# Kernel optimization log

Hardware: AMD Instinct MI355X
Metric: run time of the kernel (lower is better)

The kernel has to match this reference:

```python
import jax, jax.numpy as jnp
from jax import lax
import numpy as np

HEADS = 3
DIM_HEAD = 64
INNER = HEADS * DIM_HEAD  # 192
SCALE = DIM_HEAD ** -0.5
BN_EPS = 1e-5


def _sep_conv(x, dw, gamma, beta, mean, var, pw, stride):
    """Depthwise conv (SAME) -> BatchNorm (inference) -> 1x1 pointwise conv."""
    C = x.shape[-1]
    x = lax.conv_general_dilated(
        x, dw, window_strides=(stride, stride), padding='SAME',
        dimension_numbers=('NHWC', 'HWIO', 'NHWC'), feature_group_count=C)
    x = (x - mean) * lax.rsqrt(var + BN_EPS) * gamma + beta
    return jnp.einsum('bhwc,cd->bhwd', x, pw)


def setup_inputs() -> dict:
    key = jax.random.key(0)
    ks = jax.random.split(key, 8)
    B, H, W, C = 8, 56, 56, 192
    return {
        'x': jax.random.normal(ks[0], (B, H, W, C), dtype=jnp.float32),
        'dw_q': jax.random.normal(ks[1], (3, 3, 1, C), dtype=jnp.float32) * 0.1,
        'q_gamma': jnp.ones((C,), jnp.float32),
        'q_beta': jnp.zeros((C,), jnp.float32),
        'q_mean': jnp.zeros((C,), jnp.float32),
        'q_var': jnp.ones((C,), jnp.float32),
        'pw_q': jax.random.normal(ks[2], (C, INNER), dtype=jnp.float32) / np.sqrt(C).astype(np.float32),
        'dw_kv': jax.random.normal(ks[3], (3, 3, 1, C), dtype=jnp.float32) * 0.1,
        'kv_gamma': jnp.ones((C,), jnp.float32),
        'kv_beta': jnp.zeros((C,), jnp.float32),
        'kv_mean': jnp.zeros((C,), jnp.float32),
        'kv_var': jnp.ones((C,), jnp.float32),
        'pw_kv': jax.random.normal(ks[4], (C, 2 * INNER), dtype=jnp.float32) / np.sqrt(C).astype(np.float32),
        'out_w': jax.random.normal(ks[5], (INNER, C), dtype=jnp.float32) / np.sqrt(INNER).astype(np.float32),
        'out_b': jnp.zeros((C,), jnp.float32),
    }


def reference(x, dw_q, q_gamma, q_beta, q_mean, q_var, pw_q,
              dw_kv, kv_gamma, kv_beta, kv_mean, kv_var, pw_kv,
              out_w, out_b):
    B, H, W, C = x.shape
    q = _sep_conv(x, dw_q, q_gamma, q_beta, q_mean, q_var, pw_q, 1)      # [B,H,W,INNER]
    kv = _sep_conv(x, dw_kv, kv_gamma, kv_beta, kv_mean, kv_var, pw_kv, 2)  # [B,H/2,W/2,2*INNER]
    k, v = jnp.split(kv, 2, axis=-1)

    def split_heads(t):
        b, h, w, _ = t.shape
        return t.reshape(b, h * w, HEADS, DIM_HEAD)

    q, k, v = split_heads(q), split_heads(k), split_heads(v)  # [B,N,h,d]
    scores = jnp.einsum('bihd,bjhd->bhij', q, k) * SCALE       # [B,h,Nq,Nkv]
    attn = jax.nn.softmax(scores, axis=-1)
    o = jnp.einsum('bhij,bjhd->bihd', attn, v)                 # [B,Nq,h,d]
    o = o.reshape(B, H, W, INNER)
    return jnp.einsum('bhwc,cd->bhwd', o, out_w) + out_b
```

## Files before the change

### kernel.cpp

```cpp
#include <hip/hip_runtime.h>
#include <hip/hip_bf16.h>

namespace {
constexpr int Bb = 8, Hh = 56, Ww = 56, Cc = 192;
constexpr int NQ  = Hh * Ww;
constexpr int NKV = 28 * 28;
constexpr float EPS = 1e-5f;
constexpr float QSCALE = 0.125f * 1.4426950408889634f;
}

typedef __attribute__((ext_vector_type(8))) short          bf16x8;
typedef __attribute__((ext_vector_type(4))) float          f32x4;
typedef __attribute__((ext_vector_type(8))) unsigned short u16x8;

__device__ inline unsigned short f2b(float f) {
  __hip_bfloat16 h = __float2bfloat16(f);
  return __builtin_bit_cast(unsigned short, h);
}

__device__ inline uint2 pack4(float a, float b, float c, float d) {
  uint2 r;
  r.x = (unsigned)f2b(a) | ((unsigned)f2b(b) << 16);
  r.y = (unsigned)f2b(c) | ((unsigned)f2b(d) << 16);
  return r;
}

__device__ inline void dwbn_body(
    int idx, const float* __restrict__ x, const float* __restrict__ w,
    const float* __restrict__ gamma, const float* __restrict__ beta,
    const float* __restrict__ mean, const float* __restrict__ var,
    unsigned short* __restrict__ out, int OH, int OW, int stride, int pad)
{
  int c4 = idx % 48;
  int t = idx / 48;
  int ow = t % OW; t /= OW;
  int oh = t % OH; int b = t / OH;
  const int c = c4 * 4;

  float4 acc = make_float4(0.f, 0.f, 0.f, 0.f);
#pragma unroll
  for (int kh = 0; kh < 3; ++kh) {
    int ih = oh * stride - pad + kh;
    if (ih < 0 || ih >= Hh) continue;
#pragma unroll
    for (int kw = 0; kw < 3; ++kw) {
      int iw = ow * stride - pad + kw;
      if (iw < 0 || iw >= Ww) continue;
      float4 xv = *(const float4*)&x[((size_t)(b * Hh + ih) * Ww + iw) * Cc + c];
      float4 wv = *(const float4*)&w[(kh * 3 + kw) * Cc + c];
      acc.x += xv.x * wv.x; acc.y += xv.y * wv.y;
      acc.z += xv.z * wv.z; acc.w += xv.w * wv.w;
    }
  }
  float4 gm = *(const float4*)&gamma[c];
  float4 bt = *(const float4*)&beta[c];
  float4 mn = *(const float4*)&mean[c];
  float4 vr = *(const float4*)&var[c];
  float r0 = (acc.x - mn.x) * gm.x / sqrtf(vr.x + EPS) + bt.x;
  float r1 = (acc.y - mn.y) * gm.y / sqrtf(vr.y + EPS) + bt.y;
  float r2 = (acc.z - mn.z) * gm.z / sqrtf(vr.z + EPS) + bt.z;
  float r3 = (acc.w - mn.w) * gm.w / sqrtf(vr.w + EPS) + bt.w;
  const size_t row = (size_t)(b * OH + oh) * OW + ow;
  *reinterpret_cast<uint2*>(&out[row * 192 + c]) = pack4(r0, r1, r2, r3);
}

__global__ __launch_bounds__(256) void stage1_kernel(
    const float* __restrict__ x,
    const float* __restrict__ dw_q, const float* __restrict__ q_gamma,
    const float* __restrict__ q_beta, const float* __restrict__ q_mean,
    const float* __restrict__ q_var,
    const float* __restrict__ dw_kv, const float* __restrict__ kv_gamma,
    const float* __restrict__ kv_beta, const float* __restrict__ kv_mean,
    const float* __restrict__ kv_var,
    const float* __restrict__ pwq, const float* __restrict__ pwkv,
    const float* __restrict__ outw,
    unsigned short* __restrict__ dwq, unsigned short* __restrict__ dwkv,
    unsigned short* __restrict__ wq, unsigned short* __restrict__ wkv,
    unsigned short* __restrict__ wo)
{
  const int blk = blockIdx.x;
  if (blk < 4704) {
    dwbn_body(blk * 256 + threadIdx.x, x, dw_q, q_gamma, q_beta, q_mean, q_var,
              dwq, 56, 56, 1, 1);
  } else if (blk < 5880) {
    dwbn_body((blk - 4704) * 256 + threadIdx.x, x, dw_kv, kv_gamma, kv_beta,
              kv_mean, kv_var, dwkv, 28, 28, 2, 0);
  } else {
    int i = (blk - 5880) * 256 + threadIdx.x;
    if (i < 36864) {
      int n = i / 192, k = i - n * 192;
      wq[i] = f2b(pwq[k * 192 + n]);
    } else if (i < 110592) {
      int j = i - 36864;
      int n = j / 192, k = j - n * 192;
      wkv[j] = f2b(pwkv[k * 384 + n]);
    } else {
      int j = i - 110592;
      int n = j / 192, k = j - n * 192;
      wo[j] = f2b(outw[k * 192 + n]);
    }
  }
}

__global__ __launch_bounds__(256) void gemm_qkv_kernel(
    const unsigned short* __restrict__ dwq, const unsigned short* __restrict__ dwkv,
    const unsigned short* __restrict__ Wq, const unsigned short* __restrict__ Wkv,
    unsigned short* __restrict__ Qbuf, unsigned short* __restrict__ Kbuf,
    unsigned short* __restrict__ Vtbuf)
{
  __shared__ unsigned short As[128][72];
  __shared__ unsigned short Bs[64][72];

  const int blk = blockIdx.x;
  const bool isQ = blk < 588;
  const int lb = isQ ? blk : blk - 588;
  const unsigned short* __restrict__ A  = isQ ? dwq : dwkv;
  const unsigned short* __restrict__ Bt = isQ ? Wq : Wkv;
  const int nbl = isQ ? 3 : 6;
  const int NR  = isQ ? 3136 : 784;

  const int bm = lb / nbl, bn = lb % nbl;
  const int row0 = bm << 7, col0 = bn << 6;
  const int tid = threadIdx.x;
  const int lane = tid & 63, w = tid >> 6;
  const int lr = lane & 15, lg = lane >> 4;
  const int wm = w >> 1, wn = w & 1;

  f32x4 acc[4][2];
#pragma unroll
  for (int mr = 0; mr < 4; ++mr)
#pragma unroll
    for (int nr = 0; nr < 2; ++nr) acc[mr][nr] = (f32x4){0.f, 0.f, 0.f, 0.f};

  for (int k0 = 0; k0 < 192; k0 += 64) {
    {
      const int r = tid >> 1, c0 = (tid & 1) * 32;
      const unsigned short* src = A + (size_t)(row0 + r) * 192 + k0 + c0;
#pragma unroll
      for (int u = 0; u < 4; ++u)
        *(u16x8*)&As[r][c0 + u * 8] = *(const u16x8*)&src[u * 8];
    }
    {
      const int n = tid >> 2, c0 = (tid & 3) * 16;
      const unsigned short* src = Bt + (size_t)(col0 + n) * 192 + k0 + c0;
#pragma unroll
      for (int u = 0; u < 2; ++u)
        *(u16x8*)&Bs[n][c0 + u * 8] = *(const u16x8*)&src[u * 8];
    }
    __syncthreads();
#pragma unroll
    for (int ks = 0; ks < 2; ++ks) {
      bf16x8 a[4], b[2];
#pragma unroll
      for (int mr = 0; mr < 4; ++mr)
        a[mr] = *(const bf16x8*)&As[wm * 64 + mr * 16 + lr][ks * 32 + lg * 8];
#pragma unroll
      for (int nr = 0; nr < 2; ++nr)
        b[nr] = *(const bf16x8*)&Bs[wn * 32 + nr * 16 + lr][ks * 32 + lg * 8];
#pragma unroll
      for (int mr = 0; mr < 4; ++mr)
#pragma unroll
        for (int nr = 0; nr < 2; ++nr)
          acc[mr][nr] = __builtin_amdgcn_mfma_f32_16x16x32_bf16(a[mr], b[nr], acc[mr][nr], 0, 0, 0);
    }
    __syncthreads();
  }

#pragma unroll
  for (int mr = 0; mr < 4; ++mr) {
#pragma unroll
    for (int nr = 0; nr < 2; ++nr) {
      const int c = col0 + wn * 32 + nr * 16 + lr;
      const int rbase = row0 + wm * 64 + mr * 16 + lg * 4;
      if (isQ) {
        const int h = c >> 6, d = c & 63;
        const int b = rbase / 3136;
        const int n0 = rbase - b * 3136;
#pragma unroll
        for (int j = 0; j < 4; ++j)
          Qbuf[(((size_t)b * 3 + h) * 3136 + n0 + j) * 64 + d] = f2b(acc[mr][nr][j] * QSCALE);
      } else if (c < 192) {
        const int h = c >> 6, d = c & 63;
        const int b = rbase / 784;
        const int n0 = rbase - b * 784;
#pragma unroll
        for (int j = 0; j < 4; ++j)
          Kbuf[(((size_t)b * 3 + h) * 784 + n0 + j) * 64 + d] = f2b(acc[mr][nr][j]);
      } else {
        const int h = (c - 192) >> 6, d = (c - 192) & 63;
        const int b = rbase / 784;
        const int n0 = rbase - b * 784;
        uint2 v = pack4(acc[mr][nr][0], acc[mr][nr][1], acc[mr][nr][2], acc[mr][nr][3]);
        *reinterpret_cast<uint2*>(&Vtbuf[(((size_t)b * 3 + h) * 64 + d) * 784 + n0]) = v;
      }
    }
  }
}

__global__ __launch_bounds__(256) void gemm_out_kernel(
    const unsigned short* __restrict__ A, const unsigned short* __restrict__ Bt,
    const float* __restrict__ bias, float* __restrict__ O32)
{
  __shared__ unsigned short As[128][72];
  __shared__ unsigned short Bs[64][72];

  const int bm = blockIdx.x / 3, bn = blockIdx.x % 3;
  const int row0 = bm << 7, col0 = bn << 6;
  const int tid = threadIdx.x;
  const int lane = tid & 63, w = tid >> 6;
  const int lr = lane & 15, lg = lane >> 4;
  const int wm = w >> 1, wn = w & 1;

  f32x4 acc[4][2];
#pragma unroll
  for (int mr = 0; mr < 4; ++mr)
#pragma unroll
    for (int nr = 0; nr < 2; ++nr) acc[mr][nr] = (f32x4){0.f, 0.f, 0.f, 0.f};

  for (int k0 = 0; k0 < 192; k0 += 64) {
    {
      const int r = tid >> 1, c0 = (tid & 1) * 32;
      const unsigned short* src = A + (size_t)(row0 + r) * 192 + k0 + c0;
#pragma unroll
      for (int u = 0; u < 4; ++u)
        *(u16x8*)&As[r][c0 + u * 8] = *(const u16x8*)&src[u * 8];
    }
    {
      const int n = tid >> 2, c0 = (tid & 3) * 16;
      const unsigned short* src = Bt + (size_t)(col0 + n) * 192 + k0 + c0;
#pragma unroll
      for (int u = 0; u < 2; ++u)
        *(u16x8*)&Bs[n][c0 + u * 8] = *(const u16x8*)&src[u * 8];
    }
    __syncthreads();
#pragma unroll
    for (int ks = 0; ks < 2; ++ks) {
      bf16x8 a[4], b[2];
#pragma unroll
      for (int mr = 0; mr < 4; ++mr)
        a[mr] = *(const bf16x8*)&As[wm * 64 + mr * 16 + lr][ks * 32 + lg * 8];
#pragma unroll
      for (int nr = 0; nr < 2; ++nr)
        b[nr] = *(const bf16x8*)&Bs[wn * 32 + nr * 16 + lr][ks * 32 + lg * 8];
#pragma unroll
      for (int mr = 0; mr < 4; ++mr)
#pragma unroll
        for (int nr = 0; nr < 2; ++nr)
          acc[mr][nr] = __builtin_amdgcn_mfma_f32_16x16x32_bf16(a[mr], b[nr], acc[mr][nr], 0, 0, 0);
    }
    __syncthreads();
  }

#pragma unroll
  for (int mr = 0; mr < 4; ++mr) {
#pragma unroll
    for (int nr = 0; nr < 2; ++nr) {
      const int c = col0 + wn * 32 + nr * 16 + lr;
      const int rbase = row0 + wm * 64 + mr * 16 + lg * 4;
      const float bb = bias[c];
#pragma unroll
      for (int j = 0; j < 4; ++j)
        O32[(size_t)(rbase + j) * 192 + c] = acc[mr][nr][j] + bb;
    }
  }
}

__global__ __launch_bounds__(256) void attn_mfma_kernel(
    const unsigned short* __restrict__ Qb, const unsigned short* __restrict__ Kb,
    const unsigned short* __restrict__ Vtb, unsigned short* __restrict__ Ob)
{
  __shared__ unsigned short Ks[64][72];
  __shared__ unsigned short Vts[64][72];
  __shared__ unsigned short Ps[64][72];
  __shared__ float ls[4][16];

  const int blk = blockIdx.x;
  const int qt = blk % 49;
  const int bh = blk / 49;
  const int n0 = qt * 64;
  const int tid = threadIdx.x;
  const int lane = tid & 63;
  const int w = tid >> 6;
  const int lr = lane & 15, lg = lane >> 4;
  const int srow = w * 16 + lr;
  const int scc  = lg;

  const unsigned short* qrow = Qb + ((size_t)bh * NQ + n0 + w * 16 + lr) * 64;
  const bf16x8 aq0 = *(const bf16x8*)&qrow[lg * 8];
  const bf16x8 aq1 = *(const bf16x8*)&qrow[32 + lg * 8];

  const unsigned short* kbase = Kb + (size_t)bh * NKV * 64;
  const unsigned short* vrow  = Vtb + ((size_t)bh * 64 + srow) * NKV;

  u16x8 kr0, kr1, vr0, vr1;
  {
    const unsigned short* kp = kbase + (size_t)srow * 64;
    kr0 = *(const u16x8*)&kp[scc * 8];
    kr1 = *(const u16x8*)&kp[scc * 8 + 32];
    vr0 = *(const u16x8*)&vrow[scc * 8];
    vr1 = *(const u16x8*)&vrow[scc * 8 + 32];
  }
  *(u16x8*)&Ks[srow][scc * 8]       = kr0;
  *(u16x8*)&Ks[srow][scc * 8 + 32]  = kr1;
  *(u16x8*)&Vts[srow][scc * 8]      = vr0;
  *(u16x8*)&Vts[srow][scc * 8 + 32] = vr1;
  __syncthreads();

  f32x4 oacc[4];
#pragma unroll
  for (int db = 0; db < 4; ++db) oacc[db] = (f32x4){0.f, 0.f, 0.f, 0.f};
  float lsum = 0.f;

  for (int kt = 0; kt < 12; ++kt) {
    {
      const int nk = kt + 1;
      const int kvg = (nk * 64 + srow < NKV) ? nk * 64 + srow : NKV - 1;
      const unsigned short* kp = kbase + (size_t)kvg * 64;
      kr0 = *(const u16x8*)&kp[scc * 8];
      kr1 = *(const u16x8*)&kp[scc * 8 + 32];
      const int vb = nk * 64 + scc * 8;
      const int vc0 = (vb      <= NKV - 8) ? vb      : NKV - 8;
      const int vc1 = (vb + 32 <= NKV - 8) ? vb + 32 : NKV - 8;
      vr0 = *(const u16x8*)&vrow[vc0];
      vr1 = *(const u16x8*)&vrow[vc1];
    }

    f32x4 st[4];
#pragma unroll
    for (int nb = 0; nb < 4; ++nb) {
      const bf16x8 bk0 = *(const bf16x8*)&Ks[nb * 16 + lr][lg * 8];
      const bf16x8 bk1 = *(const bf16x8*)&Ks[nb * 16 + lr][32 + lg * 8];
      f32x4 a = (f32x4){0.f, 0.f, 0.f, 0.f};
      a = __builtin_amdgcn_mfma_f32_16x16x32_bf16(bk0, aq0, a, 0, 0, 0);
      a = __builtin_amdgcn_mfma_f32_16x16x32_bf16(bk1, aq1, a, 0, 0, 0);
      st[nb] = a;
    }

#pragma unroll
    for (int nb = 0; nb < 4; ++nb) {
      float p[4];
#pragma unroll
      for (int r = 0; r < 4; ++r) p[r] = exp2f(st[nb][r]);
      lsum += (p[0] + p[1]) + (p[2] + p[3]);
      uint2 u = pack4(p[0], p[1], p[2], p[3]);
      *reinterpret_cast<uint2*>(&Ps[w * 16 + lr][nb * 16 + lg * 4]) = u;
    }

    const bf16x8 pa0 = *(const bf16x8*)&Ps[w * 16 + lr][lg * 8];
    const bf16x8 pa1 = *(const bf16x8*)&Ps[w * 16 + lr][32 + lg * 8];
#pragma unroll
    for (int db = 0; db < 4; ++db) {
      const bf16x8 vb0 = *(const bf16x8*)&Vts[db * 16 + lr][lg * 8];
      const bf16x8 vb1 = *(const bf16x8*)&Vts[db * 16 + lr][32 + lg * 8];
      oacc[db] = __builtin_amdgcn_mfma_f32_16x16x32_bf16(pa0, vb0, oacc[db], 0, 0, 0);
      oacc[db] = __builtin_amdgcn_mfma_f32_16x16x32_bf16(pa1, vb1, oacc[db], 0, 0, 0);
    }

    __syncthreads();
    *(u16x8*)&Ks[srow][scc * 8]       = kr0;
    *(u16x8*)&Ks[srow][scc * 8 + 32]  = kr1;
    *(u16x8*)&Vts[srow][scc * 8]      = vr0;
    *(u16x8*)&Vts[srow][scc * 8 + 32] = vr1;
    __syncthreads();
  }

  {
    const bf16x8 bk0 = *(const bf16x8*)&Ks[lr][lg * 8];
    const bf16x8 bk1 = *(const bf16x8*)&Ks[lr][32 + lg * 8];
    f32x4 a = (f32x4){0.f, 0.f, 0.f, 0.f};
    a = __builtin_amdgcn_mfma_f32_16x16x32_bf16(bk0, aq0, a, 0, 0, 0);
    a = __builtin_amdgcn_mfma_f32_16x16x32_bf16(bk1, aq1, a, 0, 0, 0);
    float p[4];
#pragma unroll
    for (int r = 0; r < 4; ++r) p[r] = exp2f(a[r]);
    lsum += (p[0] + p[1]) + (p[2] + p[3]);
    *reinterpret_cast<uint2*>(&Ps[w * 16 + lr][lg * 4]) = pack4(p[0], p[1], p[2], p[3]);
    uint2 z; z.x = 0u; z.y = 0u;
    *reinterpret_cast<uint2*>(&Ps[w * 16 + lr][16 + lg * 4]) = z;
    const bf16x8 pa0 = *(const bf16x8*)&Ps[w * 16 + lr][lg * 8];
#pragma unroll
    for (int db = 0; db < 4; ++db) {
      const bf16x8 vb0 = *(const bf16x8*)&Vts[db * 16 + lr][lg * 8];
      oacc[db] = __builtin_amdgcn_mfma_f32_16x16x32_bf16(pa0, vb0, oacc[db], 0, 0, 0);
    }
  }

  float l = lsum;
  l += __shfl_xor(l, 16);
  l += __shfl_xor(l, 32);
  if (lg == 0) ls[w][lr] = l;
  const float4 lv = *(const float4*)&ls[w][lg * 4];

  const int b = bh / 3, h = bh - b * 3;
  float linv[4];
#pragma unroll
  for (int j = 0; j < 4; ++j) linv[j] = 1.f / ((&lv.x)[j]);
#pragma unroll
  for (int j = 0; j < 4; ++j) {
    const int qg = n0 + w * 16 + lg * 4 + j;
    unsigned short* orow = Ob + ((size_t)b * NQ + qg) * 192 + h * 64 + lr;
#pragma unroll
    for (int db = 0; db < 4; ++db) orow[db * 16] = f2b(oacc[db][j] * linv[j]);
  }
}

extern "C" void kernel_launch(void* const* d_in, const int* in_sizes, int n_in,
                              void* d_out, int out_size, void* d_ws, size_t ws_size,
                              hipStream_t stream)
{
  const float* x        = (const float*)d_in[0];
  const float* dw_q     = (const float*)d_in[1];
  const float* q_gamma  = (const float*)d_in[2];
  const float* q_beta   = (const float*)d_in[3];
  const float* q_mean   = (const float*)d_in[4];
  const float* q_var    = (const float*)d_in[5];
  const float* pw_q     = (const float*)d_in[6];
  const float* dw_kv    = (const float*)d_in[7];
  const float* kv_gamma = (const float*)d_in[8];
  const float* kv_beta  = (const float*)d_in[9];
  const float* kv_mean  = (const float*)d_in[10];
  const float* kv_var   = (const float*)d_in[11];
  const float* pw_kv    = (const float*)d_in[12];
  const float* out_w    = (const float*)d_in[13];
  const float* out_b    = (const float*)d_in[14];
  float* out = (float*)d_out;

  unsigned short* dwq   = (unsigned short*)d_ws;
  unsigned short* dwkv  = dwq   + (size_t)25088 * 192;
  unsigned short* Qbuf  = dwkv  + (size_t)6272 * 192;
  unsigned short* Kbuf  = Qbuf  + (size_t)24 * 3136 * 64;
  unsigned short* Vtbuf = Kbuf  + (size_t)24 * 784 * 64;
  unsigned short* Wq    = Vtbuf + (size_t)24 * 784 * 64;
  unsigned short* Wkv   = Wq + 36864;
  unsigned short* Wo    = Wkv + 73728;

  stage1_kernel<<<6456, 256, 0, stream>>>(
      x, dw_q, q_gamma, q_beta, q_mean, q_var,
      dw_kv, kv_gamma, kv_beta, kv_mean, kv_var,
      pw_q, pw_kv, out_w, dwq, dwkv, Wq, Wkv, Wo);
  gemm_qkv_kernel<<<882, 256, 0, stream>>>(dwq, dwkv, Wq, Wkv, Qbuf, Kbuf, Vtbuf);
  attn_mfma_kernel<<<8 * 3 * 49, 256, 0, stream>>>(Qbuf, Kbuf, Vtbuf, dwq);
  gemm_out_kernel<<<588, 256, 0, stream>>>(dwq, Wo, out_b, out);
}
```

Before: 89.00 us.

## Fuse depthwise conv+BN into QKV pointwise GEMM via shared-memory A tile

New measurement: 125.6 us. +41.1%, slower.

```diff
diff --git a/kernel.cpp b/kernel.cpp
--- a/kernel.cpp
+++ b/kernel.cpp
@@ -25,46 +25,28 @@
   return r;
 }
 
-__device__ inline void dwbn_body(
-    int idx, const float* __restrict__ x, const float* __restrict__ w,
-    const float* __restrict__ gamma, const float* __restrict__ beta,
-    const float* __restrict__ mean, const float* __restrict__ var,
-    unsigned short* __restrict__ out, int OH, int OW, int stride, int pad)
+__global__ __launch_bounds__(256) void prep_w_kernel(
+    const float* __restrict__ pwq, const float* __restrict__ pwkv,
+    const float* __restrict__ outw,
+    unsigned short* __restrict__ wq, unsigned short* __restrict__ wkv,
+    unsigned short* __restrict__ wo)
 {
-  int c4 = idx % 48;
-  int t = idx / 48;
-  int ow = t % OW; t /= OW;
-  int oh = t % OH; int b = t / OH;
-  const int c = c4 * 4;
-
-  float4 acc = make_float4(0.f, 0.f, 0.f, 0.f);
-#pragma unroll
-  for (int kh = 0; kh < 3; ++kh) {
-    int ih = oh * stride - pad + kh;
-    if (ih < 0 || ih >= Hh) continue;
-#pragma unroll
-    for (int kw = 0; kw < 3; ++kw) {
-      int iw = ow * stride - pad + kw;
-      if (iw < 0 || iw >= Ww) continue;
-      float4 xv = *(const float4*)&x[((size_t)(b * Hh + ih) * Ww + iw) * Cc + c];
-      float4 wv = *(const float4*)&w[(kh * 3 + kw) * Cc + c];
-      acc.x += xv.x * wv.x; acc.y += xv.y * wv.y;
-      acc.z += xv.z * wv.z; acc.w += xv.w * wv.w;
-    }
-  }
-  float4 gm = *(const float4*)&gamma[c];
-  float4 bt = *(const float4*)&beta[c];
-  float4 mn = *(const float4*)&mean[c];
-  float4 vr = *(const float4*)&var[c];
-  float r0 = (acc.x - mn.x) * gm.x / sqrtf(vr.x + EPS) + bt.x;
-  float r1 = (acc.y - mn.y) * gm.y / sqrtf(vr.y + EPS) + bt.y;
-  float r2 = (acc.z - mn.z) * gm.z / sqrtf(vr.z + EPS) + bt.z;
-  float r3 = (acc.w - mn.w) * gm.w / sqrtf(vr.w + EPS) + bt.w;
-  const size_t row = (size_t)(b * OH + oh) * OW + ow;
-  *reinterpret_cast<uint2*>(&out[row * 192 + c]) = pack4(r0, r1, r2, r3);
-}
-
-__global__ __launch_bounds__(256) void stage1_kernel(
+  int i = blockIdx.x * 256 + threadIdx.x;
+  if (i < 36864) {
+    int n = i / 192, k = i - n * 192;
+    wq[i] = f2b(pwq[k * 192 + n]);
+  } else if (i < 110592) {
+    int j = i - 36864;
+    int n = j / 192, k = j - n * 192;
+    wkv[j] = f2b(pwkv[k * 384 + n]);
+  } else if (i < 147456) {
+    int j = i - 110592;
+    int n = j / 192, k = j - n * 192;
+    wo[j] = f2b(outw[k * 192 + n]);
+  }
+}
+
+__global__ __launch_bounds__(256) void dwgemm_kernel(
     const float* __restrict__ x,
     const float* __restrict__ dw_q, const float* __restrict__ q_gamma,
     const float* __restrict__ q_beta, const float* __restrict__ q_mean,
@@ -72,126 +54,123 @@
     const float* __restrict__ dw_kv, const float* __restrict__ kv_gamma,
     const float* __restrict__ kv_beta, const float* __restrict__ kv_mean,
     const float* __restrict__ kv_var,
-    const float* __restrict__ pwq, const float* __restrict__ pwkv,
-    const float* __restrict__ outw,
-    unsigned short* __restrict__ dwq, unsigned short* __restrict__ dwkv,
-    unsigned short* __restrict__ wq, unsigned short* __restrict__ wkv,
-    unsigned short* __restrict__ wo)
-{
-  const int blk = blockIdx.x;
-  if (blk < 4704) {
-    dwbn_body(blk * 256 + threadIdx.x, x, dw_q, q_gamma, q_beta, q_mean, q_var,
-              dwq, 56, 56, 1, 1);
-  } else if (blk < 5880) {
-    dwbn_body((blk - 4704) * 256 + threadIdx.x, x, dw_kv, kv_gamma, kv_beta,
-              kv_mean, kv_var, dwkv, 28, 28, 2, 0);
-  } else {
-    int i = (blk - 5880) * 256 + threadIdx.x;
-    if (i < 36864) {
-      int n = i / 192, k = i - n * 192;
-      wq[i] = f2b(pwq[k * 192 + n]);
-    } else if (i < 110592) {
-      int j = i - 36864;
-      int n = j / 192, k = j - n * 192;
-      wkv[j] = f2b(pwkv[k * 384 + n]);
-    } else {
-      int j = i - 110592;
-      int n = j / 192, k = j - n * 192;
-      wo[j] = f2b(outw[k * 192 + n]);
-    }
-  }
-}
-
-__global__ __launch_bounds__(256) void gemm_qkv_kernel(
-    const unsigned short* __restrict__ dwq, const unsigned short* __restrict__ dwkv,
     const unsigned short* __restrict__ Wq, const unsigned short* __restrict__ Wkv,
     unsigned short* __restrict__ Qbuf, unsigned short* __restrict__ Kbuf,
     unsigned short* __restrict__ Vtbuf)
 {
-  __shared__ unsigned short As[128][72];
-  __shared__ unsigned short Bs[64][72];
+  __shared__ unsigned short As[64][200];
+  __shared__ unsigned short Bs[192][72];
 
   const int blk = blockIdx.x;
-  const bool isQ = blk < 588;
-  const int lb = isQ ? blk : blk - 588;
-  const unsigned short* __restrict__ A  = isQ ? dwq : dwkv;
-  const unsigned short* __restrict__ Bt = isQ ? Wq : Wkv;
-  const int nbl = isQ ? 3 : 6;
-  const int NR  = isQ ? 3136 : 784;
-
-  const int bm = lb / nbl, bn = lb % nbl;
-  const int row0 = bm << 7, col0 = bn << 6;
+  const bool isQ = blk < 392;
+  const int lb = isQ ? blk : blk - 392;
+  const int bn = isQ ? 0 : lb / 98;
+  const int row0 = (isQ ? lb : (lb % 98)) * 64;
+
+  const float* dww = isQ ? dw_q : dw_kv;
+  const float* gmp = isQ ? q_gamma : kv_gamma;
+  const float* btp = isQ ? q_beta  : kv_beta;
+  const float* mnp = isQ ? q_mean  : kv_mean;
+  const float* vrp = isQ ? q_var   : kv_var;
+  const unsigned short* Btw = isQ ? Wq : (Wkv + (size_t)bn * 192 * 192);
+  const int OH = isQ ? 56 : 28, OW = isQ ? 56 : 28;
+  const int stride = isQ ? 1 : 2, pad = isQ ? 1 : 0;
+  const int NR = isQ ? 3136 : 784;
+
   const int tid = threadIdx.x;
+
+#pragma unroll
+  for (int it = 0; it < 12; ++it) {
+    const int task = it * 256 + tid;
+    const int c4 = task % 48, r = task / 48;
+    const int p = row0 + r;
+    const int b = p / NR;
+    const int rem = p - b * NR;
+    const int oh = rem / OW, ow = rem - oh * OW;
+    const int c = c4 * 4;
+
+    float4 acc = make_float4(0.f, 0.f, 0.f, 0.f);
+#pragma unroll
+    for (int kh = 0; kh < 3; ++kh) {
+      const int ih = oh * stride - pad + kh;
+      if (ih < 0 || ih >= Hh) continue;
+#pragma unroll
+      for (int kw = 0; kw < 3; ++kw) {
+        const int iw = ow * stride - pad + kw;
+        if (iw < 0 || iw >= Ww) continue;
+        float4 xv = *(const float4*)&x[((size_t)(b * Hh + ih) * Ww + iw) * Cc + c];
+        float4 wv = *(const float4*)&dww[(kh * 3 + kw) * Cc + c];
+        acc.x += xv.x * wv.x; acc.y += xv.y * wv.y;
+        acc.z += xv.z * wv.z; acc.w += xv.w * wv.w;
+      }
+    }
+    float4 gm = *(const float4*)&gmp[c];
+    float4 bt = *(const float4*)&btp[c];
+    float4 mn = *(const float4*)&mnp[c];
+    float4 vr = *(const float4*)&vrp[c];
+    float r0 = (acc.x - mn.x) * gm.x / sqrtf(vr.x + EPS) + bt.x;
+    float r1 = (acc.y - mn.y) * gm.y / sqrtf(vr.y + EPS) + bt.y;
+    float r2 = (acc.z - mn.z) * gm.z / sqrtf(vr.z + EPS) + bt.z;
+    float r3 = (acc.w - mn.w) * gm.w / sqrtf(vr.w + EPS) + bt.w;
+    *reinterpret_cast<uint2*>(&As[r][c]) = pack4(r0, r1, r2, r3);
+  }
+
   const int lane = tid & 63, w = tid >> 6;
   const int lr = lane & 15, lg = lane >> 4;
   const int wm = w >> 1, wn = w & 1;
 
-  f32x4 acc[4][2];
-#pragma unroll
-  for (int mr = 0; mr < 4; ++mr)
-#pragma unroll
-    for (int nr = 0; nr < 2; ++nr) acc[mr][nr] = (f32x4){0.f, 0.f, 0.f, 0.f};
+  f32x4 acc[2][6];
+#pragma unroll
+  for (int mr = 0; mr < 2; ++mr)
+#pragma unroll
+    for (int nr = 0; nr < 6; ++nr) acc[mr][nr] = (f32x4){0.f, 0.f, 0.f, 0.f};
 
   for (int k0 = 0; k0 < 192; k0 += 64) {
-    {
-      const int r = tid >> 1, c0 = (tid & 1) * 32;
-      const unsigned short* src = A + (size_t)(row0 + r) * 192 + k0 + c0;
-#pragma unroll
-      for (int u = 0; u < 4; ++u)
-        *(u16x8*)&As[r][c0 + u * 8] = *(const u16x8*)&src[u * 8];
-    }
-    {
-      const int n = tid >> 2, c0 = (tid & 3) * 16;
-      const unsigned short* src = Bt + (size_t)(col0 + n) * 192 + k0 + c0;
-#pragma unroll
-      for (int u = 0; u < 2; ++u)
-        *(u16x8*)&Bs[n][c0 + u * 8] = *(const u16x8*)&src[u * 8];
+    __syncthreads();
+#pragma unroll
+    for (int it = 0; it < 6; ++it) {
+      const int task = it * 256 + tid;
+      const int n = task >> 3, c8 = task & 7;
+      *(u16x8*)&Bs[n][c8 * 8] = *(const u16x8*)&Btw[(size_t)n * 192 + k0 + c8 * 8];
     }
     __syncthreads();
 #pragma unroll
     for (int ks = 0; ks < 2; ++ks) {
-      bf16x8 a[4], b[2];
-#pragma unroll
-      for (int mr = 0; mr < 4; ++mr)
-        a[mr] = *(const bf16x8*)&As[wm * 64 + mr * 16 + lr][ks * 32 + lg * 8];
-#pragma unroll
-      for (int nr = 0; nr < 2; ++nr)
-        b[nr] = *(const bf16x8*)&Bs[wn * 32 + nr * 16 + lr][ks * 32 + lg * 8];
-#pragma unroll
-      for (int mr = 0; mr < 4; ++mr)
-#pragma unroll
-        for (int nr = 0; nr < 2; ++nr)
+      bf16x8 a[2], b[6];
+#pragma unroll
+      for (int mr = 0; mr < 2; ++mr)
+        a[mr] = *(const bf16x8*)&As[wm * 32 + mr * 16 + lr][k0 + ks * 32 + lg * 8];
+#pragma unroll
+      for (int nr = 0; nr < 6; ++nr)
+        b[nr] = *(const bf16x8*)&Bs[wn * 96 + nr * 16 + lr][ks * 32 + lg * 8];
+#pragma unroll
+      for (int mr = 0; mr < 2; ++mr)
+#pragma unroll
+        for (int nr = 0; nr < 6; ++nr)
           acc[mr][nr] = __builtin_amdgcn_mfma_f32_16x16x32_bf16(a[mr], b[nr], acc[mr][nr], 0, 0, 0);
     }
-    __syncthreads();
-  }
-
-#pragma unroll
-  for (int mr = 0; mr < 4; ++mr) {
-#pragma unroll
-    for (int nr = 0; nr < 2; ++nr) {
-      const int c = col0 + wn * 32 + nr * 16 + lr;
-      const int rbase = row0 + wm * 64 + mr * 16 + lg * 4;
+  }
+
+#pragma unroll
+  for (int mr = 0; mr < 2; ++mr) {
+#pragma unroll
+    for (int nr = 0; nr < 6; ++nr) {
+      const int c = wn * 96 + nr * 16 + lr;
+      const int rbase = row0 + wm * 32 + mr * 16 + lg * 4;
+      const int h = c >> 6, d = c & 63;
+      const int b = rbase / NR;
+      const int n0r = rbase - b * NR;
       if (isQ) {
-        const int h = c >> 6, d = c & 63;
-        const int b = rbase / 3136;
-        const int n0 = rbase - b * 3136;
 #pragma unroll
         for (int j = 0; j < 4; ++j)
-          Qbuf[(((size_t)b * 3 + h) * 3136 + n0 + j) * 64 + d] = f2b(acc[mr][nr][j] * QSCALE);
-      } else if (c < 192) {
-        const int h = c >> 6, d = c & 63;
-        const int b = rbase / 784;
-        const int n0 = rbase - b * 784;
+          Qbuf[(((size_t)b * 3 + h) * 3136 + n0r + j) * 64 + d] = f2b(acc[mr][nr][j] * QSCALE);
+      } else if (bn == 0) {
 #pragma unroll
         for (int j = 0; j < 4; ++j)
-          Kbuf[(((size_t)b * 3 + h) * 784 + n0 + j) * 64 + d] = f2b(acc[mr][nr][j]);
+          Kbuf[(((size_t)b * 3 + h) * 784 + n0r + j) * 64 + d] = f2b(acc[mr][nr][j]);
       } else {
-        const int h = (c - 192) >> 6, d = (c - 192) & 63;
-        const int b = rbase / 784;
-        const int n0 = rbase - b * 784;
         uint2 v = pack4(acc[mr][nr][0], acc[mr][nr][1], acc[mr][nr][2], acc[mr][nr][3]);
-        *reinterpret_cast<uint2*>(&Vtbuf[(((size_t)b * 3 + h) * 64 + d) * 784 + n0]) = v;
+        *reinterpret_cast<uint2*>(&Vtbuf[(((size_t)b * 3 + h) * 64 + d) * 784 + n0r]) = v;
       }
     }
   }
@@ -425,20 +404,19 @@
   const float* out_b    = (const float*)d_in[14];
   float* out = (float*)d_out;
 
-  unsigned short* dwq   = (unsigned short*)d_ws;
-  unsigned short* dwkv  = dwq   + (size_t)25088 * 192;
-  unsigned short* Qbuf  = dwkv  + (size_t)6272 * 192;
+  unsigned short* Obuf  = (unsigned short*)d_ws;
+  unsigned short* Qbuf  = Obuf  + (size_t)25088 * 192;
   unsigned short* Kbuf  = Qbuf  + (size_t)24 * 3136 * 64;
   unsigned short* Vtbuf = Kbuf  + (size_t)24 * 784 * 64;
   unsigned short* Wq    = Vtbuf + (size_t)24 * 784 * 64;
   unsigned short* Wkv   = Wq + 36864;
   unsigned short* Wo    = Wkv + 73728;
 
-  stage1_kernel<<<6456, 256, 0, stream>>>(
+  prep_w_kernel<<<576, 256, 0, stream>>>(pw_q, pw_kv, out_w, Wq, Wkv, Wo);
+  dwgemm_kernel<<<588, 256, 0, stream>>>(
       x, dw_q, q_gamma, q_beta, q_mean, q_var,
       dw_kv, kv_gamma, kv_beta, kv_mean, kv_var,
-      pw_q, pw_kv, out_w, dwq, dwkv, Wq, Wkv, Wo);
-  gemm_qkv_kernel<<<882, 256, 0, stream>>>(dwq, dwkv, Wq, Wkv, Qbuf, Kbuf, Vtbuf);
-  attn_mfma_kernel<<<8 * 3 * 49, 256, 0, stream>>>(Qbuf, Kbuf, Vtbuf, dwq);
-  gemm_out_kernel<<<588, 256, 0, stream>>>(dwq, Wo, out_b, out);
-}
+      Wq, Wkv, Qbuf, Kbuf, Vtbuf);
+  attn_mfma_kernel<<<8 * 3 * 49, 256, 0, stream>>>(Qbuf, Kbuf, Vtbuf, Obuf);
+  gemm_out_kernel<<<588, 256, 0, stream>>>(Obuf, Wo, out_b, out);
+}
```

## Process 128 queries per attention block to reuse K/V tiles across two row groups

Applied to the files above, without the earlier changes.

Measured after the change: 91.45 us. +2.7%, slower.

```diff
diff --git a/kernel.cpp b/kernel.cpp
--- a/kernel.cpp
+++ b/kernel.cpp
@@ -271,13 +271,13 @@
 {
   __shared__ unsigned short Ks[64][72];
   __shared__ unsigned short Vts[64][72];
-  __shared__ unsigned short Ps[64][72];
-  __shared__ float ls[4][16];
+  __shared__ unsigned short Ps[128][72];
+  __shared__ float ls[4][2][16];
 
   const int blk = blockIdx.x;
-  const int qt = blk % 49;
-  const int bh = blk / 49;
-  const int n0 = qt * 64;
+  const int qt = blk % 25;
+  const int bh = blk / 25;
+  const int n0 = qt * 128;
   const int tid = threadIdx.x;
   const int lane = tid & 63;
   const int w = tid >> 6;
@@ -285,9 +285,14 @@
   const int srow = w * 16 + lr;
   const int scc  = lg;
 
-  const unsigned short* qrow = Qb + ((size_t)bh * NQ + n0 + w * 16 + lr) * 64;
-  const bf16x8 aq0 = *(const bf16x8*)&qrow[lg * 8];
-  const bf16x8 aq1 = *(const bf16x8*)&qrow[32 + lg * 8];
+  const int qrA = n0 + w * 32 + lr;
+  const int qrB = qrA + 16;
+  const unsigned short* qpA = Qb + ((size_t)bh * NQ + (qrA < NQ ? qrA : NQ - 1)) * 64;
+  const unsigned short* qpB = Qb + ((size_t)bh * NQ + (qrB < NQ ? qrB : NQ - 1)) * 64;
+  const bf16x8 qa0 = *(const bf16x8*)&qpA[lg * 8];
+  const bf16x8 qa1 = *(const bf16x8*)&qpA[32 + lg * 8];
+  const bf16x8 qb0 = *(const bf16x8*)&qpB[lg * 8];
+  const bf16x8 qb1 = *(const bf16x8*)&qpB[32 + lg * 8];
 
   const unsigned short* kbase = Kb + (size_t)bh * NKV * 64;
   const unsigned short* vrow  = Vtb + ((size_t)bh * 64 + srow) * NKV;
@@ -306,10 +311,16 @@
   *(u16x8*)&Vts[srow][scc * 8 + 32] = vr1;
   __syncthreads();
 
-  f32x4 oacc[4];
-#pragma unroll
-  for (int db = 0; db < 4; ++db) oacc[db] = (f32x4){0.f, 0.f, 0.f, 0.f};
-  float lsum = 0.f;
+  f32x4 oaccA[4], oaccB[4];
+#pragma unroll
+  for (int db = 0; db < 4; ++db) {
+    oaccA[db] = (f32x4){0.f, 0.f, 0.f, 0.f};
+    oaccB[db] = (f32x4){0.f, 0.f, 0.f, 0.f};
+  }
+  float lsumA = 0.f, lsumB = 0.f;
+
+  const int rowA = w * 32 + lr;
+  const int rowB = rowA + 16;
 
   for (int kt = 0; kt < 12; ++kt) {
     {
@@ -325,35 +336,44 @@
       vr1 = *(const u16x8*)&vrow[vc1];
     }
 
-    f32x4 st[4];
+    f32x4 stA[4], stB[4];
 #pragma unroll
     for (int nb = 0; nb < 4; ++nb) {
       const bf16x8 bk0 = *(const bf16x8*)&Ks[nb * 16 + lr][lg * 8];
       const bf16x8 bk1 = *(const bf16x8*)&Ks[nb * 16 + lr][32 + lg * 8];
       f32x4 a = (f32x4){0.f, 0.f, 0.f, 0.f};
-      a = __builtin_amdgcn_mfma_f32_16x16x32_bf16(bk0, aq0, a, 0, 0, 0);
-      a = __builtin_amdgcn_mfma_f32_16x16x32_bf16(bk1, aq1, a, 0, 0, 0);
-      st[nb] = a;
+      a = __builtin_amdgcn_mfma_f32_16x16x32_bf16(bk0, qa0, a, 0, 0, 0);
+      a = __builtin_amdgcn_mfma_f32_16x16x32_bf16(bk1, qa1, a, 0, 0, 0);
+      stA[nb] = a;
+      f32x4 b = (f32x4){0.f, 0.f, 0.f, 0.f};
+      b = __builtin_amdgcn_mfma_f32_16x16x32_bf16(bk0, qb0, b, 0, 0, 0);
+      b = __builtin_amdgcn_mfma_f32_16x16x32_bf16(bk1, qb1, b, 0, 0, 0);
+      stB[nb] = b;
     }
 
 #pragma unroll
     for (int nb = 0; nb < 4; ++nb) {
-      float p[4];
-#pragma unroll
-      for (int r = 0; r < 4; ++r) p[r] = exp2f(st[nb][r]);
-      lsum += (p[0] + p[1]) + (p[2] + p[3]);
-      uint2 u = pack4(p[0], p[1], p[2], p[3]);
-      *reinterpret_cast<uint2*>(&Ps[w * 16 + lr][nb * 16 + lg * 4]) = u;
-    }
-
-    const bf16x8 pa0 = *(const bf16x8*)&Ps[w * 16 + lr][lg * 8];
-    const bf16x8 pa1 = *(const bf16x8*)&Ps[w * 16 + lr][32 + lg * 8];
+      float pA[4], pB[4];
+#pragma unroll
+      for (int r = 0; r < 4; ++r) { pA[r] = exp2f(stA[nb][r]); pB[r] = exp2f(stB[nb][r]); }
+      lsumA += (pA[0] + pA[1]) + (pA[2] + pA[3]);
+      lsumB += (pB[0] + pB[1]) + (pB[2] + pB[3]);
+      *reinterpret_cast<uint2*>(&Ps[rowA][nb * 16 + lg * 4]) = pack4(pA[0], pA[1], pA[2], pA[3]);
+      *reinterpret_cast<uint2*>(&Ps[rowB][nb * 16 + lg * 4]) = pack4(pB[0], pB[1], pB[2], pB[3]);
+    }
+
+    const bf16x8 paA0 = *(const bf16x8*)&Ps[rowA][lg * 8];
+    const bf16x8 paA1 = *(const bf16x8*)&Ps[rowA][32 + lg * 8];
+    const bf16x8 paB0 = *(const bf16x8*)&Ps[rowB][lg * 8];
+    const bf16x8 paB1 = *(const bf16x8*)&Ps[rowB][32 + lg * 8];
 #pragma unroll
     for (int db = 0; db < 4; ++db) {
       const bf16x8 vb0 = *(const bf16x8*)&Vts[db * 16 + lr][lg * 8];
       const bf16x8 vb1 = *(const bf16x8*)&Vts[db * 16 + lr][32 + lg * 8];
-      oacc[db] = __builtin_amdgcn_mfma_f32_16x16x32_bf16(pa0, vb0, oacc[db], 0, 0, 0);
-      oacc[db] = __builtin_amdgcn_mfma_f32_16x16x32_bf16(pa1, vb1, oacc[db], 0, 0, 0);
+      oaccA[db] = __builtin_amdgcn_mfma_f32_16x16x32_bf16(paA0, vb0, oaccA[db], 0, 0, 0);
+      oaccA[db] = __builtin_amdgcn_mfma_f32_16x16x32_bf16(paA1, vb1, oaccA[db], 0, 0, 0);
+      oaccB[db] = __builtin_amdgcn_mfma_f32_16x16x32_bf16(paB0, vb0, oaccB[db], 0, 0, 0);
+      oaccB[db] = __builtin_amdgcn_mfma_f32_16x16x32_bf16(paB1, vb1, oaccB[db], 0, 0, 0);
     }
 
     __syncthreads();
@@ -368,39 +388,58 @@
     const bf16x8 bk0 = *(const bf16x8*)&Ks[lr][lg * 8];
     const bf16x8 bk1 = *(const bf16x8*)&Ks[lr][32 + lg * 8];
     f32x4 a = (f32x4){0.f, 0.f, 0.f, 0.f};
-    a = __builtin_amdgcn_mfma_f32_16x16x32_bf16(bk0, aq0, a, 0, 0, 0);
-    a = __builtin_amdgcn_mfma_f32_16x16x32_bf16(bk1, aq1, a, 0, 0, 0);
-    float p[4];
-#pragma unroll
-    for (int r = 0; r < 4; ++r) p[r] = exp2f(a[r]);
-    lsum += (p[0] + p[1]) + (p[2] + p[3]);
-    *reinterpret_cast<uint2*>(&Ps[w * 16 + lr][lg * 4]) = pack4(p[0], p[1], p[2], p[3]);
+    a = __builtin_amdgcn_mfma_f32_16x16x32_bf16(bk0, qa0, a, 0, 0, 0);
+    a = __builtin_amdgcn_mfma_f32_16x16x32_bf16(bk1, qa1, a, 0, 0, 0);
+    f32x4 b = (f32x4){0.f, 0.f, 0.f, 0.f};
+    b = __builtin_amdgcn_mfma_f32_16x16x32_bf16(bk0, qb0, b, 0, 0, 0);
+    b = __builtin_amdgcn_mfma_f32_16x16x32_bf16(bk1, qb1, b, 0, 0, 0);
+    float pA[4], pB[4];
+#pragma unroll
+    for (int r = 0; r < 4; ++r) { pA[r] = exp2f(a[r]); pB[r] = exp2f(b[r]); }
+    lsumA += (pA[0] + pA[1]) + (pA[2] + pA[3]);
+    lsumB += (pB[0] + pB[1]) + (pB[2] + pB[3]);
+    *reinterpret_cast<uint2*>(&Ps[rowA][lg * 4]) = pack4(pA[0], pA[1], pA[2], pA[3]);
+    *reinterpret_cast<uint2*>(&Ps[rowB][lg * 4]) = pack4(pB[0], pB[1], pB[2], pB[3]);
     uint2 z; z.x = 0u; z.y = 0u;
-    *reinterpret_cast<uint2*>(&Ps[w * 16 + lr][16 + lg * 4]) = z;
-    const bf16x8 pa0 = *(const bf16x8*)&Ps[w * 16 + lr][lg * 8];
+    *reinterpret_cast<uint2*>(&Ps[rowA][16 + lg * 4]) = z;
+    *reinterpret_cast<uint2*>(&Ps[rowB][16 + lg * 4]) = z;
+    const bf16x8 paA0 = *(const bf16x8*)&Ps[rowA][lg * 8];
+    const bf16x8 paB0 = *(const bf16x8*)&Ps[rowB][lg * 8];
 #pragma unroll
     for (int db = 0; db < 4; ++db) {
       const bf16x8 vb0 = *(const bf16x8*)&Vts[db * 16 + lr][lg * 8];
-      oacc[db] = __builtin_amdgcn_mfma_f32_16x16x32_bf16(pa0, vb0, oacc[db], 0, 0, 0);
-    }
-  }
-
-  float l = lsum;
-  l += __shfl_xor(l, 16);
-  l += __shfl_xor(l, 32);
-  if (lg == 0) ls[w][lr] = l;
-  const float4 lv = *(const float4*)&ls[w][lg * 4];
+      oaccA[db] = __builtin_amdgcn_mfma_f32_16x16x32_bf16(paA0, vb0, oaccA[db], 0, 0, 0);
+      oaccB[db] = __builtin_amdgcn_mfma_f32_16x16x32_bf16(paB0, vb0, oaccB[db], 0, 0, 0);
+    }
+  }
+
+  float lA = lsumA;
+  lA += __shfl_xor(lA, 16);
+  lA += __shfl_xor(lA, 32);
+  float lB = lsumB;
+  lB += __shfl_xor(lB, 16);
+  lB += __shfl_xor(lB, 32);
+  if (lg == 0) { ls[w][0][lr] = lA; ls[w][1][lr] = lB; }
+  const float4 lvA = *(const float4*)&ls[w][0][lg * 4];
+  const float4 lvB = *(const float4*)&ls[w][1][lg * 4];
 
   const int b = bh / 3, h = bh - b * 3;
-  float linv[4];
-#pragma unroll
-  for (int j = 0; j < 4; ++j) linv[j] = 1.f / ((&lv.x)[j]);
 #pragma unroll
   for (int j = 0; j < 4; ++j) {
-    const int qg = n0 + w * 16 + lg * 4 + j;
-    unsigned short* orow = Ob + ((size_t)b * NQ + qg) * 192 + h * 64 + lr;
-#pragma unroll
-    for (int db = 0; db < 4; ++db) orow[db * 16] = f2b(oacc[db][j] * linv[j]);
+    const int qgA = n0 + w * 32 + lg * 4 + j;
+    if (qgA < NQ) {
+      const float inv = 1.f / ((&lvA.x)[j]);
+      unsigned short* orow = Ob + ((size_t)b * NQ + qgA) * 192 + h * 64 + lr;
+#pragma unroll
+      for (int db = 0; db < 4; ++db) orow[db * 16] = f2b(oaccA[db][j] * inv);
+    }
+    const int qgB = qgA + 16;
+    if (qgB < NQ) {
+      const float inv = 1.f / ((&lvB.x)[j]);
+      unsigned short* orow = Ob + ((size_t)b * NQ + qgB) * 192 + h * 64 + lr;
+#pragma unroll
+      for (int db = 0; db < 4; ++db) orow[db * 16] = f2b(oaccB[db][j] * inv);
+    }
   }
 }
 
@@ -439,6 +478,6 @@
       dw_kv, kv_gamma, kv_beta, kv_mean, kv_var,
       pw_q, pw_kv, out_w, dwq, dwkv, Wq, Wkv, Wo);
   gemm_qkv_kernel<<<882, 256, 0, stream>>>(dwq, dwkv, Wq, Wkv, Qbuf, Kbuf, Vtbuf);
-  attn_mfma_kernel<<<8 * 3 * 49, 256, 0, stream>>>(Qbuf, Kbuf, Vtbuf, dwq);
+  attn_mfma_kernel<<<24 * 25, 256, 0, stream>>>(Qbuf, Kbuf, Vtbuf, dwq);
   gemm_out_kernel<<<588, 256, 0, stream>>>(dwq, Wo, out_b, out);
 }
```
